# Performance work log

Measured on AMD Instinct MI355X. Metric: run time of the kernel, lower is better.

The kernel has to match this reference:

```python
import jax, jax.numpy as jnp
import numpy as np


def rotary_pos_emb(x):
    # x: [b, h, l, k]; interleaved rotary embedding (pairs are (0,1),(2,3),...)
    dim = x.shape[-1]
    seq = x.shape[-2]
    ts = jnp.arange(0, dim, 2, dtype=jnp.float32)
    inv_freqs = 10000.0 ** (-ts / dim)                      # [dim/2]
    grid = jnp.arange(seq, dtype=jnp.float32)[:, None] * inv_freqs[None, :]  # [l, dim/2]
    sin_embs = jnp.repeat(jnp.sin(grid), 2, axis=-1)[None]  # [1, l, dim] (interleaved repeat)
    cos_embs = jnp.repeat(jnp.cos(grid), 2, axis=-1)[None]
    x1, x2 = x[..., ::2], x[..., 1::2]
    xs = jnp.stack([-x2, x1], axis=-1).reshape(x.shape)     # interleave (-x2, x1)
    return x * cos_embs + xs * sin_embs


def setup_inputs() -> dict:
    key = jax.random.key(0)
    ks = jax.random.split(key, 5)
    b, l, d = 2, 2048, 1024
    scale = 1.0 / np.sqrt(d)
    return {
        "x": jax.random.normal(ks[0], (b, l, d), dtype=jnp.float32),
        "Wq": jax.random.normal(ks[1], (d, d), dtype=jnp.float32) * scale,
        "Wk": jax.random.normal(ks[2], (d, d), dtype=jnp.float32) * scale,
        "Wv": jax.random.normal(ks[3], (d, d), dtype=jnp.float32) * scale,
        "Wo": jax.random.normal(ks[4], (d, d), dtype=jnp.float32) * scale,
        "is_training": 0,
    }


def reference(x, Wq, Wk, Wv, Wo, is_training):
    n_heads = 16
    b, l, d = x.shape
    k_size = d // n_heads
    # NOTE: module scales q by 1/sqrt(model_size), not 1/sqrt(key_size)
    q = (x @ Wq) / jnp.sqrt(jnp.float32(d))
    q = q.reshape(b, l, n_heads, k_size).transpose(0, 2, 1, 3)  # b h l k
    k = (x @ Wk).reshape(b, l, n_heads, k_size).transpose(0, 2, 1, 3)
    v = (x @ Wv).reshape(b, l, n_heads, k_size).transpose(0, 2, 1, 3)
    q = rotary_pos_emb(q)
    k = rotary_pos_emb(k)
    logits = jnp.einsum('bhik,bhjk->bhij', q, k)  # no mask, no dropout (eval)
    a = jax.nn.softmax(logits, axis=-1)
    y = jnp.einsum('bhij,bhjv->bhiv', a, v)
    y = y.transpose(0, 2, 1, 3).reshape(b, l, d)  # b l (h v)
    return y @ Wo
```

## Files before the change

kernel.cpp:

```cpp
#include <hip/hip_runtime.h>
#include <stdint.h>

typedef unsigned short u16;
using short8 = __attribute__((ext_vector_type(8))) short;
using f32x4  = __attribute__((ext_vector_type(4))) float;

typedef __attribute__((address_space(1))) unsigned int gu32;
typedef __attribute__((address_space(3))) unsigned int lu32;

__device__ __forceinline__ void gl2lds16(const u16* g, u16* lds_wave_base) {
    __builtin_amdgcn_global_load_lds(
        (gu32*)(uintptr_t)(const void*)g,
        (lu32*)(uint32_t)(uintptr_t)(void*)lds_wave_base,
        16, 0, 0);
}

__device__ inline float bf2f(u16 u) {
    union { unsigned int i; float f; } v;
    v.i = ((unsigned int)u) << 16;
    return v.f;
}
__device__ inline u16 f2bf(float f) {
    union { float f; unsigned int i; } v;
    v.f = f;
    unsigned int x = v.i;
    return (u16)((x + 0x7fffu + ((x >> 16) & 1u)) >> 16);
}
__device__ inline u16 f2bf_trunc(float f) {
    union { float f; unsigned int i; } v;
    v.f = f;
    return (u16)(v.i >> 16);
}

__global__ __launch_bounds__(256) void cvt_x(const float* __restrict__ x,
                                             u16* __restrict__ xb)
{
    int i = (blockIdx.x * 256 + threadIdx.x) * 4;
    float4 v = *(const float4*)(x + i);
    ushort4 o;
    o.x = f2bf(v.x); o.y = f2bf(v.y); o.z = f2bf(v.z); o.w = f2bf(v.w);
    *(ushort4*)(xb + i) = o;
}

__global__ __launch_bounds__(256) void rope_tab(float2* __restrict__ tab)
{
    int idx = blockIdx.x * 256 + threadIdx.x;
    int pos = idx >> 5, pi = idx & 31;
    const float l2_10000_over_32 = 0.41524101186f;
    float ang = (float)pos * __builtin_amdgcn_exp2f(-(float)pi * l2_10000_over_32);
    float sn, cs;
    __sincosf(ang, &sn, &cs);
    tab[idx] = make_float2(cs, sn);
}

__global__ __launch_bounds__(256) void transpose4_cvt(
    const float* __restrict__ w0, const float* __restrict__ w1,
    const float* __restrict__ w2, const float* __restrict__ w3,
    u16* __restrict__ t0, u16* __restrict__ t1,
    u16* __restrict__ t2, u16* __restrict__ t3)
{
    __shared__ u16 tile[32][33];
    const float* src; u16* dst;
    switch (blockIdx.z) {
        case 0:  src = w0; dst = t0; break;
        case 1:  src = w1; dst = t1; break;
        case 2:  src = w2; dst = t2; break;
        default: src = w3; dst = t3; break;
    }
    int tx = threadIdx.x, ty = threadIdx.y;
    int c0 = blockIdx.x * 32, r0 = blockIdx.y * 32;
    #pragma unroll
    for (int i = 0; i < 4; i++)
        tile[ty + i * 8][tx] = f2bf(src[(size_t)(r0 + ty + i * 8) * 1024 + c0 + tx]);
    __syncthreads();
    #pragma unroll
    for (int i = 0; i < 4; i++)
        dst[(size_t)(c0 + ty + i * 8) * 1024 + r0 + tx] = tile[tx][ty + i * 8];
}

__global__ __launch_bounds__(256) void transpose_v(const u16* __restrict__ Vb,
                                                   u16* __restrict__ VT)
{
    __shared__ u16 t[32][33];
    int bh = blockIdx.z, b = bh >> 4, h = bh & 15;
    int p0 = blockIdx.x * 32, c0 = blockIdx.y * 32;
    int tx = threadIdx.x, ty = threadIdx.y;
    #pragma unroll
    for (int i = 0; i < 4; i++)
        t[ty + i * 8][tx] = Vb[(size_t)(b * 2048 + p0 + ty + i * 8) * 1024 + h * 64 + c0 + tx];
    __syncthreads();
    #pragma unroll
    for (int i = 0; i < 4; i++)
        VT[((size_t)bh * 64 + c0 + ty + i * 8) * 2048 + p0 + tx] = t[tx][ty + i * 8];
}

__global__ __launch_bounds__(256) void gemm_qkv(
    const u16* __restrict__ A, const u16* __restrict__ Bt,
    const float2* __restrict__ ropetab,
    u16* __restrict__ Qb, u16* __restrict__ Kb, u16* __restrict__ Vb)
{
    __shared__ __align__(16) u16 As[128 * 32];
    __shared__ __align__(16) u16 Bs[128 * 32];
    __shared__ float2 scs[128 * 33];

    const int tid  = threadIdx.x;
    const int lane = tid & 63;
    const int wid  = tid >> 6;
    const int quad = lane >> 4;
    const int l15  = lane & 15;
    const int wm   = wid >> 1, wn = wid & 1;

    const int m0 = blockIdx.y * 128;
    const int n0 = blockIdx.x * 128;
    const int mat = n0 >> 10;
    const int ln0 = n0 & 1023;
    u16* C = (mat == 0) ? Qb : (mat == 1 ? Kb : Vb);

    if (mat < 2) {
        int pos0 = m0 & 2047;
        #pragma unroll
        for (int t = 0; t < 16; t++) {
            int idx = t * 256 + tid;
            int rr = idx >> 5, pp = idx & 31;
            scs[rr * 33 + pp] = ropetab[(size_t)(pos0 + rr) * 32 + pp];
        }
    }

    f32x4 acc[4][4] = {};

    for (int k0 = 0; k0 < 1024; k0 += 32) {
        #pragma unroll
        for (int it = 0; it < 2; it++) {
            int c   = it * 256 + tid;
            int row = c >> 2;
            int col = ((c & 3) ^ (row & 3)) * 8;
            u16* lbA = &As[(size_t)(it * 256 + wid * 64) * 8];
            u16* lbB = &Bs[(size_t)(it * 256 + wid * 64) * 8];
            gl2lds16(&A [(size_t)(m0 + row) * 1024 + k0 + col], lbA);
            gl2lds16(&Bt[(size_t)(n0 + row) * 1024 + k0 + col], lbB);
        }
        __syncthreads();

        short8 a[4], b[4];
        #pragma unroll
        for (int i = 0; i < 4; i++) {
            int ra = wm * 64 + i * 16 + l15;
            int rb = wn * 64 + i * 16 + l15;
            a[i] = *(const short8*)(&As[ra * 32 + ((quad ^ (ra & 3)) * 8)]);
            b[i] = *(const short8*)(&Bs[rb * 32 + ((quad ^ (rb & 3)) * 8)]);
        }
        #pragma unroll
        for (int i = 0; i < 4; i++)
            #pragma unroll
            for (int j = 0; j < 4; j++)
                acc[i][j] = __builtin_amdgcn_mfma_f32_16x16x32_bf16(a[i], b[j], acc[i][j], 0, 0, 0);
        __syncthreads();
    }

    const float scale = (mat == 0) ? (0.03125f * 1.44269504f) : 1.0f;
    const bool do_rope = (mat < 2);
    const int odd = l15 & 1;

    #pragma unroll
    for (int i = 0; i < 4; i++)
        #pragma unroll
        for (int j = 0; j < 4; j++)
            #pragma unroll
            for (int r = 0; r < 4; r++) {
                int lrow = wm * 64 + i * 16 + quad * 4 + r;
                int col  = ln0 + wn * 64 + j * 16 + l15;
                float v = acc[i][j][r] * scale;
                float outv;
                if (do_rope) {
                    float vp = __shfl_xor(v, 1);
                    int pi   = (col & 63) >> 1;
                    float2 sc = scs[lrow * 33 + pi];
                    outv = odd ? (v * sc.x + vp * sc.y) : (v * sc.x - vp * sc.y);
                } else {
                    outv = v;
                }
                C[(size_t)(m0 + lrow) * 1024 + col] = f2bf(outv);
            }
}

__global__ __launch_bounds__(256) void gemm_out(
    const u16* __restrict__ A, const u16* __restrict__ Bt, float* __restrict__ C)
{
    __shared__ __align__(16) u16 As[128 * 32];
    __shared__ __align__(16) u16 Bs[128 * 32];

    const int tid  = threadIdx.x;
    const int lane = tid & 63;
    const int wid  = tid >> 6;
    const int quad = lane >> 4;
    const int l15  = lane & 15;
    const int wm   = wid >> 1, wn = wid & 1;

    const int m0 = blockIdx.y * 128;
    const int n0 = blockIdx.x * 128;

    f32x4 acc[4][4] = {};

    for (int k0 = 0; k0 < 1024; k0 += 32) {
        #pragma unroll
        for (int it = 0; it < 2; it++) {
            int c   = it * 256 + tid;
            int row = c >> 2;
            int col = ((c & 3) ^ (row & 3)) * 8;
            u16* lbA = &As[(size_t)(it * 256 + wid * 64) * 8];
            u16* lbB = &Bs[(size_t)(it * 256 + wid * 64) * 8];
            gl2lds16(&A [(size_t)(m0 + row) * 1024 + k0 + col], lbA);
            gl2lds16(&Bt[(size_t)(n0 + row) * 1024 + k0 + col], lbB);
        }
        __syncthreads();

        short8 a[4], b[4];
        #pragma unroll
        for (int i = 0; i < 4; i++) {
            int ra = wm * 64 + i * 16 + l15;
            int rb = wn * 64 + i * 16 + l15;
            a[i] = *(const short8*)(&As[ra * 32 + ((quad ^ (ra & 3)) * 8)]);
            b[i] = *(const short8*)(&Bs[rb * 32 + ((quad ^ (rb & 3)) * 8)]);
        }
        #pragma unroll
        for (int i = 0; i < 4; i++)
            #pragma unroll
            for (int j = 0; j < 4; j++)
                acc[i][j] = __builtin_amdgcn_mfma_f32_16x16x32_bf16(a[i], b[j], acc[i][j], 0, 0, 0);
        __syncthreads();
    }

    #pragma unroll
    for (int i = 0; i < 4; i++)
        #pragma unroll
        for (int j = 0; j < 4; j++)
            #pragma unroll
            for (int r = 0; r < 4; r++) {
                int row = m0 + wm * 64 + i * 16 + quad * 4 + r;
                int col = n0 + wn * 64 + j * 16 + l15;
                C[(size_t)row * 1024 + col] = acc[i][j][r];
            }
}

__global__ __launch_bounds__(512) void attn(
    const u16* __restrict__ Q, const u16* __restrict__ Kb,
    const u16* __restrict__ VT, u16* __restrict__ Y)
{
    __shared__ __align__(16) u16 Ks [128 * 64];
    __shared__ __align__(16) u16 VTs[64 * 128];
    __shared__ __align__(16) u16 Ps [8][16 * 64];

    const int tid  = threadIdx.x;
    const int lane = tid & 63, wid = tid >> 6;
    const int quad = lane >> 4, l15 = lane & 15;

    const int bh = blockIdx.x;
    const int qt = blockIdx.y;
    const int bb = bh >> 4, h = bh & 15;

    const size_t base = ((size_t)bb * 2048) * 1024 + (size_t)h * 64;

    short8 qf[2];
    {
        size_t qrow = (size_t)qt * 128 + wid * 16 + l15;
        const u16* qp = Q + base + qrow * 1024;
        qf[0] = *(const short8*)(qp + quad * 8);
        qf[1] = *(const short8*)(qp + 32 + quad * 8);
    }

    f32x4 o[4] = {};
    float l_r[4] = {0.f, 0.f, 0.f, 0.f};

    for (int j0 = 0; j0 < 2048; j0 += 128) {
        __syncthreads();
        #pragma unroll
        for (int it = 0; it < 2; it++) {
            int c = it * 512 + tid;
            int rk = c >> 3, ck = ((c & 7)  ^ (rk & 7))  * 8;
            int rv = c >> 4, cv = ((c & 15) ^ (rv & 15)) * 8;
            u16* lbK = &Ks [(size_t)(it * 512 + wid * 64) * 8];
            u16* lbV = &VTs[(size_t)(it * 512 + wid * 64) * 8];
            gl2lds16(&Kb[base + (size_t)(j0 + rk) * 1024 + ck], lbK);
            gl2lds16(&VT[((size_t)bh * 64 + rv) * 2048 + j0 + cv], lbV);
        }
        __syncthreads();

        f32x4 s[8];
        #pragma unroll
        for (int nt = 0; nt < 8; nt++) {
            int R = nt * 16 + l15;
            short8 k0 = *(const short8*)(&Ks[R * 64 + (( quad      ^ (R & 7)) * 8)]);
            short8 k1 = *(const short8*)(&Ks[R * 64 + (((quad + 4) ^ (R & 7)) * 8)]);
            f32x4 z = {};
            z = __builtin_amdgcn_mfma_f32_16x16x32_bf16(qf[0], k0, z, 0, 0, 0);
            z = __builtin_amdgcn_mfma_f32_16x16x32_bf16(qf[1], k1, z, 0, 0, 0);
            s[nt] = z;
        }

        #pragma unroll
        for (int hh = 0; hh < 2; hh++) {
            #pragma unroll
            for (int n4 = 0; n4 < 4; n4++) {
                int nt = hh * 4 + n4;
                #pragma unroll
                for (int r = 0; r < 4; r++) {
                    float p = __builtin_amdgcn_exp2f(s[nt][r]);
                    l_r[r] += p;
                    int m = quad * 4 + r;
                    int col = n4 * 16 + l15;
                    Ps[wid][m * 64 + (((col >> 3) ^ (m & 7)) * 8) + (col & 7)]
                        = f2bf_trunc(p);
                }
            }
            asm volatile("s_waitcnt lgkmcnt(0)" ::: "memory");

            short8 pa0 = *(const short8*)(&Ps[wid][l15 * 64 + (( quad      ^ (l15 & 7)) * 8)]);
            short8 pa1 = *(const short8*)(&Ps[wid][l15 * 64 + (((quad + 4) ^ (l15 & 7)) * 8)]);
            #pragma unroll
            for (int nt = 0; nt < 4; nt++) {
                int R = nt * 16 + l15;
                short8 vb0 = *(const short8*)(&VTs[R * 128 + (((hh * 8 + quad)     ^ (R & 15)) * 8)]);
                short8 vb1 = *(const short8*)(&VTs[R * 128 + (((hh * 8 + quad + 4) ^ (R & 15)) * 8)]);
                o[nt] = __builtin_amdgcn_mfma_f32_16x16x32_bf16(pa0, vb0, o[nt], 0, 0, 0);
                o[nt] = __builtin_amdgcn_mfma_f32_16x16x32_bf16(pa1, vb1, o[nt], 0, 0, 0);
            }
            asm volatile("" ::: "memory");
        }
    }

    #pragma unroll
    for (int r = 0; r < 4; r++) {
        l_r[r] += __shfl_xor(l_r[r], 1);
        l_r[r] += __shfl_xor(l_r[r], 2);
        l_r[r] += __shfl_xor(l_r[r], 4);
        l_r[r] += __shfl_xor(l_r[r], 8);
        l_r[r] = 1.0f / l_r[r];
    }

    size_t qrow0 = (size_t)qt * 128 + wid * 16;
    #pragma unroll
    for (int nt = 0; nt < 4; nt++)
        #pragma unroll
        for (int r = 0; r < 4; r++) {
            size_t row = qrow0 + quad * 4 + r;
            Y[base + row * 1024 + nt * 16 + l15] = f2bf(o[nt][r] * l_r[r]);
        }
}

extern "C" void kernel_launch(void* const* d_in, const int* in_sizes, int n_in,
                              void* d_out, int out_size, void* d_ws, size_t ws_size,
                              hipStream_t stream)
{
    const float* x  = (const float*)d_in[0];
    const float* Wq = (const float*)d_in[1];
    const float* Wk = (const float*)d_in[2];
    const float* Wv = (const float*)d_in[3];
    const float* Wo = (const float*)d_in[4];
    float* out = (float*)d_out;

    char* ws = (char*)d_ws;
    u16*    xb    = (u16*)   (ws + (0ull  << 20));
    u16*    WqkvT = (u16*)   (ws + (8ull  << 20));
    u16*    WoT   = (u16*)   (ws + (14ull << 20));
    u16*    Qb    = (u16*)   (ws + (16ull << 20));
    u16*    Kb    = (u16*)   (ws + (24ull << 20));
    u16*    Vb    = (u16*)   (ws + (32ull << 20));
    u16*    VTb   = (u16*)   (ws + (40ull << 20));
    u16*    Yb    = (u16*)   (ws + (48ull << 20));
    float2* tab   = (float2*)(ws + (56ull << 20));

    cvt_x<<<4096, 256, 0, stream>>>(x, xb);
    rope_tab<<<256, 256, 0, stream>>>(tab);
    transpose4_cvt<<<dim3(32, 32, 4), dim3(32, 8), 0, stream>>>(
        Wq, Wk, Wv, Wo,
        WqkvT, WqkvT + (1024ull * 1024), WqkvT + (2048ull * 1024), WoT);
    gemm_qkv<<<dim3(24, 32), 256, 0, stream>>>(xb, WqkvT, tab, Qb, Kb, Vb);
    transpose_v<<<dim3(64, 2, 32), dim3(32, 8), 0, stream>>>(Vb, VTb);
    attn<<<dim3(32, 16), 512, 0, stream>>>(Qb, Kb, VTb, Yb);
    gemm_out<<<dim3(8, 32), 256, 0, stream>>>(Yb, WoT, out);
}
```

Measured before the change: 205.8 us.

## Merge prep kernels, fuse V transpose into QKV GEMM, widen GEMM K-tile

The x conversion, rope table build and weight transposes are merged into one prep launch. The separate V transpose kernel is removed: the QKV GEMM now transposes V through shared memory and writes VT directly. Both GEMMs move from a K-tile of 32 to 64 with an 8-way swizzle, which halves the barrier count. The rope epilogue now reads the table straight from global memory instead of staging it in LDS. Attention gives each half-iteration its own P buffer, which lets a compiler barrier be dropped. The trade-off is fewer launches and less memory traffic against larger LDS use per block.

```diff
diff --git a/kernel.cpp b/kernel.cpp
--- a/kernel.cpp
+++ b/kernel.cpp
@@ -32,42 +32,47 @@
     return (u16)(v.i >> 16);
 }
 
-__global__ __launch_bounds__(256) void cvt_x(const float* __restrict__ x,
-                                             u16* __restrict__ xb)
-{
-    int i = (blockIdx.x * 256 + threadIdx.x) * 4;
-    float4 v = *(const float4*)(x + i);
-    ushort4 o;
-    o.x = f2bf(v.x); o.y = f2bf(v.y); o.z = f2bf(v.z); o.w = f2bf(v.w);
-    *(ushort4*)(xb + i) = o;
-}
-
-__global__ __launch_bounds__(256) void rope_tab(float2* __restrict__ tab)
-{
-    int idx = blockIdx.x * 256 + threadIdx.x;
-    int pos = idx >> 5, pi = idx & 31;
-    const float l2_10000_over_32 = 0.41524101186f;
-    float ang = (float)pos * __builtin_amdgcn_exp2f(-(float)pi * l2_10000_over_32);
-    float sn, cs;
-    __sincosf(ang, &sn, &cs);
-    tab[idx] = make_float2(cs, sn);
-}
-
-__global__ __launch_bounds__(256) void transpose4_cvt(
+__global__ __launch_bounds__(256) void prep(
+    const float* __restrict__ x, u16* __restrict__ xb,
     const float* __restrict__ w0, const float* __restrict__ w1,
     const float* __restrict__ w2, const float* __restrict__ w3,
     u16* __restrict__ t0, u16* __restrict__ t1,
-    u16* __restrict__ t2, u16* __restrict__ t3)
-{
+    u16* __restrict__ t2, u16* __restrict__ t3,
+    float2* __restrict__ tab)
+{
+    int tx = threadIdx.x, ty = threadIdx.y;
+    int tid = ty * 32 + tx;
+    int z = blockIdx.z;
+    if (z == 4) {
+        int bidx = blockIdx.y * 32 + blockIdx.x;
+        if (bidx < 256) {
+            int idx = bidx * 256 + tid;
+            int pos = idx >> 5, pi = idx & 31;
+            const float l2_10000_over_32 = 0.41524101186f;
+            float ang = (float)pos *
+                __builtin_amdgcn_exp2f(-(float)pi * l2_10000_over_32);
+            float sn, cs;
+            __sincosf(ang, &sn, &cs);
+            tab[idx] = make_float2(cs, sn);
+        }
+        return;
+    }
+    if (z >= 5) {
+        int i = (((z - 5) * 1024 + blockIdx.y * 32 + blockIdx.x) * 256 + tid) * 4;
+        float4 v = *(const float4*)(x + i);
+        ushort4 o;
+        o.x = f2bf(v.x); o.y = f2bf(v.y); o.z = f2bf(v.z); o.w = f2bf(v.w);
+        *(ushort4*)(xb + i) = o;
+        return;
+    }
     __shared__ u16 tile[32][33];
     const float* src; u16* dst;
-    switch (blockIdx.z) {
+    switch (z) {
         case 0:  src = w0; dst = t0; break;
         case 1:  src = w1; dst = t1; break;
         case 2:  src = w2; dst = t2; break;
         default: src = w3; dst = t3; break;
     }
-    int tx = threadIdx.x, ty = threadIdx.y;
     int c0 = blockIdx.x * 32, r0 = blockIdx.y * 32;
     #pragma unroll
     for (int i = 0; i < 4; i++)
@@ -78,30 +83,14 @@
         dst[(size_t)(c0 + ty + i * 8) * 1024 + r0 + tx] = tile[tx][ty + i * 8];
 }
 
-__global__ __launch_bounds__(256) void transpose_v(const u16* __restrict__ Vb,
-                                                   u16* __restrict__ VT)
-{
-    __shared__ u16 t[32][33];
-    int bh = blockIdx.z, b = bh >> 4, h = bh & 15;
-    int p0 = blockIdx.x * 32, c0 = blockIdx.y * 32;
-    int tx = threadIdx.x, ty = threadIdx.y;
-    #pragma unroll
-    for (int i = 0; i < 4; i++)
-        t[ty + i * 8][tx] = Vb[(size_t)(b * 2048 + p0 + ty + i * 8) * 1024 + h * 64 + c0 + tx];
-    __syncthreads();
-    #pragma unroll
-    for (int i = 0; i < 4; i++)
-        VT[((size_t)bh * 64 + c0 + ty + i * 8) * 2048 + p0 + tx] = t[tx][ty + i * 8];
-}
-
 __global__ __launch_bounds__(256) void gemm_qkv(
     const u16* __restrict__ A, const u16* __restrict__ Bt,
     const float2* __restrict__ ropetab,
-    u16* __restrict__ Qb, u16* __restrict__ Kb, u16* __restrict__ Vb)
-{
-    __shared__ __align__(16) u16 As[128 * 32];
-    __shared__ __align__(16) u16 Bs[128 * 32];
-    __shared__ float2 scs[128 * 33];
+    u16* __restrict__ Qb, u16* __restrict__ Kb, u16* __restrict__ VT)
+{
+    __shared__ __align__(16) char smem[128 * 136 * 2];
+    u16* As = (u16*)smem;
+    u16* Bs = (u16*)(smem + 16384);
 
     const int tid  = threadIdx.x;
     const int lane = tid & 63;
@@ -114,26 +103,15 @@
     const int n0 = blockIdx.x * 128;
     const int mat = n0 >> 10;
     const int ln0 = n0 & 1023;
-    u16* C = (mat == 0) ? Qb : (mat == 1 ? Kb : Vb);
-
-    if (mat < 2) {
-        int pos0 = m0 & 2047;
-        #pragma unroll
-        for (int t = 0; t < 16; t++) {
-            int idx = t * 256 + tid;
-            int rr = idx >> 5, pp = idx & 31;
-            scs[rr * 33 + pp] = ropetab[(size_t)(pos0 + rr) * 32 + pp];
-        }
-    }
 
     f32x4 acc[4][4] = {};
 
-    for (int k0 = 0; k0 < 1024; k0 += 32) {
-        #pragma unroll
-        for (int it = 0; it < 2; it++) {
+    for (int k0 = 0; k0 < 1024; k0 += 64) {
+        #pragma unroll
+        for (int it = 0; it < 4; it++) {
             int c   = it * 256 + tid;
-            int row = c >> 2;
-            int col = ((c & 3) ^ (row & 3)) * 8;
+            int row = c >> 3;
+            int col = ((c & 7) ^ (row & 7)) * 8;
             u16* lbA = &As[(size_t)(it * 256 + wid * 64) * 8];
             u16* lbB = &Bs[(size_t)(it * 256 + wid * 64) * 8];
             gl2lds16(&A [(size_t)(m0 + row) * 1024 + k0 + col], lbA);
@@ -141,53 +119,78 @@
         }
         __syncthreads();
 
-        short8 a[4], b[4];
-        #pragma unroll
-        for (int i = 0; i < 4; i++) {
-            int ra = wm * 64 + i * 16 + l15;
-            int rb = wn * 64 + i * 16 + l15;
-            a[i] = *(const short8*)(&As[ra * 32 + ((quad ^ (ra & 3)) * 8)]);
-            b[i] = *(const short8*)(&Bs[rb * 32 + ((quad ^ (rb & 3)) * 8)]);
-        }
+        #pragma unroll
+        for (int s = 0; s < 2; s++) {
+            short8 a[4], b[4];
+            #pragma unroll
+            for (int i = 0; i < 4; i++) {
+                int ra = wm * 64 + i * 16 + l15;
+                int rb = wn * 64 + i * 16 + l15;
+                a[i] = *(const short8*)(&As[ra * 64 + (((s * 4 + quad) ^ (ra & 7)) * 8)]);
+                b[i] = *(const short8*)(&Bs[rb * 64 + (((s * 4 + quad) ^ (rb & 7)) * 8)]);
+            }
+            #pragma unroll
+            for (int i = 0; i < 4; i++)
+                #pragma unroll
+                for (int j = 0; j < 4; j++)
+                    acc[i][j] = __builtin_amdgcn_mfma_f32_16x16x32_bf16(a[i], b[j], acc[i][j], 0, 0, 0);
+        }
+        __syncthreads();
+    }
+
+    if (mat < 2) {
+        u16* C = (mat == 0) ? Qb : Kb;
+        const float scale = (mat == 0) ? (0.03125f * 1.44269504f) : 1.0f;
+        const int odd = l15 & 1;
         #pragma unroll
         for (int i = 0; i < 4; i++)
             #pragma unroll
             for (int j = 0; j < 4; j++)
-                acc[i][j] = __builtin_amdgcn_mfma_f32_16x16x32_bf16(a[i], b[j], acc[i][j], 0, 0, 0);
-        __syncthreads();
-    }
-
-    const float scale = (mat == 0) ? (0.03125f * 1.44269504f) : 1.0f;
-    const bool do_rope = (mat < 2);
-    const int odd = l15 & 1;
-
-    #pragma unroll
-    for (int i = 0; i < 4; i++)
-        #pragma unroll
-        for (int j = 0; j < 4; j++)
-            #pragma unroll
-            for (int r = 0; r < 4; r++) {
-                int lrow = wm * 64 + i * 16 + quad * 4 + r;
-                int col  = ln0 + wn * 64 + j * 16 + l15;
-                float v = acc[i][j][r] * scale;
-                float outv;
-                if (do_rope) {
+                #pragma unroll
+                for (int r = 0; r < 4; r++) {
+                    int lrow = wm * 64 + i * 16 + quad * 4 + r;
+                    int col  = ln0 + wn * 64 + j * 16 + l15;
+                    int pos  = (m0 + lrow) & 2047;
+                    float v  = acc[i][j][r] * scale;
                     float vp = __shfl_xor(v, 1);
-                    int pi   = (col & 63) >> 1;
-                    float2 sc = scs[lrow * 33 + pi];
-                    outv = odd ? (v * sc.x + vp * sc.y) : (v * sc.x - vp * sc.y);
-                } else {
-                    outv = v;
+                    float2 sc = ropetab[pos * 32 + ((col & 63) >> 1)];
+                    float outv = odd ? (v * sc.x + vp * sc.y)
+                                     : (v * sc.x - vp * sc.y);
+                    C[(size_t)(m0 + lrow) * 1024 + col] = f2bf(outv);
                 }
-                C[(size_t)(m0 + lrow) * 1024 + col] = f2bf(outv);
-            }
+    } else {
+        u16* T = (u16*)smem;
+        __syncthreads();
+        #pragma unroll
+        for (int i = 0; i < 4; i++)
+            #pragma unroll
+            for (int j = 0; j < 4; j++)
+                #pragma unroll
+                for (int r = 0; r < 4; r++) {
+                    int lrow = wm * 64 + i * 16 + quad * 4 + r;
+                    int lcol = wn * 64 + j * 16 + l15;
+                    T[lcol * 136 + lrow] = f2bf(acc[i][j][r]);
+                }
+        __syncthreads();
+        int bb2 = m0 >> 11, pos0 = m0 & 2047;
+        #pragma unroll
+        for (int itc = 0; itc < 8; itc++) {
+            int c  = itc * 256 + tid;
+            int ch = c >> 4;
+            int px = (c & 15) * 8;
+            int head = (ln0 + ch) >> 6;
+            size_t dst = ((size_t)(bb2 * 16 + head) * 64 + (ch & 63)) * 2048
+                         + pos0 + px;
+            *(uint4*)(&VT[dst]) = *(const uint4*)(&T[ch * 136 + px]);
+        }
+    }
 }
 
 __global__ __launch_bounds__(256) void gemm_out(
     const u16* __restrict__ A, const u16* __restrict__ Bt, float* __restrict__ C)
 {
-    __shared__ __align__(16) u16 As[128 * 32];
-    __shared__ __align__(16) u16 Bs[128 * 32];
+    __shared__ __align__(16) u16 As[128 * 64];
+    __shared__ __align__(16) u16 Bs[128 * 64];
 
     const int tid  = threadIdx.x;
     const int lane = tid & 63;
@@ -201,12 +204,12 @@
 
     f32x4 acc[4][4] = {};
 
-    for (int k0 = 0; k0 < 1024; k0 += 32) {
-        #pragma unroll
-        for (int it = 0; it < 2; it++) {
+    for (int k0 = 0; k0 < 1024; k0 += 64) {
+        #pragma unroll
+        for (int it = 0; it < 4; it++) {
             int c   = it * 256 + tid;
-            int row = c >> 2;
-            int col = ((c & 3) ^ (row & 3)) * 8;
+            int row = c >> 3;
+            int col = ((c & 7) ^ (row & 7)) * 8;
             u16* lbA = &As[(size_t)(it * 256 + wid * 64) * 8];
             u16* lbB = &Bs[(size_t)(it * 256 + wid * 64) * 8];
             gl2lds16(&A [(size_t)(m0 + row) * 1024 + k0 + col], lbA);
@@ -214,19 +217,22 @@
         }
         __syncthreads();
 
-        short8 a[4], b[4];
-        #pragma unroll
-        for (int i = 0; i < 4; i++) {
-            int ra = wm * 64 + i * 16 + l15;
-            int rb = wn * 64 + i * 16 + l15;
-            a[i] = *(const short8*)(&As[ra * 32 + ((quad ^ (ra & 3)) * 8)]);
-            b[i] = *(const short8*)(&Bs[rb * 32 + ((quad ^ (rb & 3)) * 8)]);
-        }
-        #pragma unroll
-        for (int i = 0; i < 4; i++)
-            #pragma unroll
-            for (int j = 0; j < 4; j++)
-                acc[i][j] = __builtin_amdgcn_mfma_f32_16x16x32_bf16(a[i], b[j], acc[i][j], 0, 0, 0);
+        #pragma unroll
+        for (int s = 0; s < 2; s++) {
+            short8 a[4], b[4];
+            #pragma unroll
+            for (int i = 0; i < 4; i++) {
+                int ra = wm * 64 + i * 16 + l15;
+                int rb = wn * 64 + i * 16 + l15;
+                a[i] = *(const short8*)(&As[ra * 64 + (((s * 4 + quad) ^ (ra & 7)) * 8)]);
+                b[i] = *(const short8*)(&Bs[rb * 64 + (((s * 4 + quad) ^ (rb & 7)) * 8)]);
+            }
+            #pragma unroll
+            for (int i = 0; i < 4; i++)
+                #pragma unroll
+                for (int j = 0; j < 4; j++)
+                    acc[i][j] = __builtin_amdgcn_mfma_f32_16x16x32_bf16(a[i], b[j], acc[i][j], 0, 0, 0);
+        }
         __syncthreads();
     }
 
@@ -248,7 +254,7 @@
 {
     __shared__ __align__(16) u16 Ks [128 * 64];
     __shared__ __align__(16) u16 VTs[64 * 128];
-    __shared__ __align__(16) u16 Ps [8][16 * 64];
+    __shared__ __align__(16) u16 Ps [16][16 * 64];
 
     const int tid  = threadIdx.x;
     const int lane = tid & 63, wid = tid >> 6;
@@ -299,6 +305,7 @@
 
         #pragma unroll
         for (int hh = 0; hh < 2; hh++) {
+            u16* ps = Ps[wid * 2 + hh];
             #pragma unroll
             for (int n4 = 0; n4 < 4; n4++) {
                 int nt = hh * 4 + n4;
@@ -308,14 +315,14 @@
                     l_r[r] += p;
                     int m = quad * 4 + r;
                     int col = n4 * 16 + l15;
-                    Ps[wid][m * 64 + (((col >> 3) ^ (m & 7)) * 8) + (col & 7)]
+                    ps[m * 64 + (((col >> 3) ^ (m & 7)) * 8) + (col & 7)]
                         = f2bf_trunc(p);
                 }
             }
             asm volatile("s_waitcnt lgkmcnt(0)" ::: "memory");
 
-            short8 pa0 = *(const short8*)(&Ps[wid][l15 * 64 + (( quad      ^ (l15 & 7)) * 8)]);
-            short8 pa1 = *(const short8*)(&Ps[wid][l15 * 64 + (((quad + 4) ^ (l15 & 7)) * 8)]);
+            short8 pa0 = *(const short8*)(&ps[l15 * 64 + (( quad      ^ (l15 & 7)) * 8)]);
+            short8 pa1 = *(const short8*)(&ps[l15 * 64 + (((quad + 4) ^ (l15 & 7)) * 8)]);
             #pragma unroll
             for (int nt = 0; nt < 4; nt++) {
                 int R = nt * 16 + l15;
@@ -324,7 +331,6 @@
                 o[nt] = __builtin_amdgcn_mfma_f32_16x16x32_bf16(pa0, vb0, o[nt], 0, 0, 0);
                 o[nt] = __builtin_amdgcn_mfma_f32_16x16x32_bf16(pa1, vb1, o[nt], 0, 0, 0);
             }
-            asm volatile("" ::: "memory");
         }
     }
 
@@ -364,18 +370,14 @@
     u16*    WoT   = (u16*)   (ws + (14ull << 20));
     u16*    Qb    = (u16*)   (ws + (16ull << 20));
     u16*    Kb    = (u16*)   (ws + (24ull << 20));
-    u16*    Vb    = (u16*)   (ws + (32ull << 20));
-    u16*    VTb   = (u16*)   (ws + (40ull << 20));
-    u16*    Yb    = (u16*)   (ws + (48ull << 20));
-    float2* tab   = (float2*)(ws + (56ull << 20));
-
-    cvt_x<<<4096, 256, 0, stream>>>(x, xb);
-    rope_tab<<<256, 256, 0, stream>>>(tab);
-    transpose4_cvt<<<dim3(32, 32, 4), dim3(32, 8), 0, stream>>>(
-        Wq, Wk, Wv, Wo,
-        WqkvT, WqkvT + (1024ull * 1024), WqkvT + (2048ull * 1024), WoT);
-    gemm_qkv<<<dim3(24, 32), 256, 0, stream>>>(xb, WqkvT, tab, Qb, Kb, Vb);
-    transpose_v<<<dim3(64, 2, 32), dim3(32, 8), 0, stream>>>(Vb, VTb);
+    u16*    VTb   = (u16*)   (ws + (32ull << 20));
+    u16*    Yb    = (u16*)   (ws + (40ull << 20));
+    float2* tab   = (float2*)(ws + (48ull << 20));
+
+    prep<<<dim3(32, 32, 9), dim3(32, 8), 0, stream>>>(
+        x, xb, Wq, Wk, Wv, Wo,
+        WqkvT, WqkvT + (1024ull * 1024), WqkvT + (2048ull * 1024), WoT, tab);
+    gemm_qkv<<<dim3(24, 32), 256, 0, stream>>>(xb, WqkvT, tab, Qb, Kb, VTb);
     attn<<<dim3(32, 16), 512, 0, stream>>>(Qb, Kb, VTb, Yb);
     gemm_out<<<dim3(8, 32), 256, 0, stream>>>(Yb, WoT, out);
 }
```

Result: no change. 205.3 us (-0.2%).
